# Kernel optimization log

Hardware: AMD Instinct MI355X
Metric: run time of the kernel (lower is better)

Reference implementation:

```python
import jax, jax.numpy as jnp
import numpy as np

B, N, E = 64, 2048, 32768
F_IN, NHID, RULES = 256, 512, 128
RATIO = 0.5
K1 = int(np.ceil(RATIO * N)); K2 = int(np.ceil(RATIO * K1)); K3 = int(np.ceil(RATIO * K2))


def _gcn(x, src, dst, em, W, b):
    # GCNConv with self-loops and symmetric normalization; em is a float edge-validity mask.
    n = x.shape[0]
    h = x @ W  # [n, out]
    deg = jax.ops.segment_sum(em, dst, num_segments=n) + 1.0  # in-degree + self-loop
    dinv = jax.lax.rsqrt(deg)
    coef = dinv[src] * dinv[dst] * em  # [E]
    agg = jax.ops.segment_sum(h[src] * coef[:, None], dst, num_segments=n)
    return agg + h / deg[:, None] + b  # second term = self-loop with norm 1/deg


def _sag_pool(x, src, dst, em, Wg, bg, k):
    # SAGPooling: GCN scorer, per-graph top-k, scale kept nodes by tanh(score), filter+reindex edges.
    n = x.shape[0]
    score = _gcn(x, src, dst, em, Wg, bg)[:, 0]  # [n]
    vals, perm = jax.lax.top_k(score, k)
    xk = x[perm] * jnp.tanh(vals)[:, None]  # [k, F]
    newidx = jnp.full((n,), -1, dtype=src.dtype).at[perm].set(jnp.arange(k, dtype=src.dtype))
    ns, nd = newidx[src], newidx[dst]
    keep = em * (ns >= 0).astype(em.dtype) * (nd >= 0).astype(em.dtype)
    return xk, jnp.maximum(ns, 0), jnp.maximum(nd, 0), keep


_gcn_b = jax.vmap(_gcn, in_axes=(0, 0, 0, 0, None, None))
_pool_b = jax.vmap(_sag_pool, in_axes=(0, 0, 0, 0, None, None, None))


def setup_inputs() -> dict:
    key = jax.random.key(0)
    ks = jax.random.split(key, 16)
    def w(k, shape, fan_in):
        return jax.random.normal(k, shape, jnp.float32) * (1.0 / np.sqrt(fan_in))
    return {
        "x": jax.random.normal(ks[0], (B, N, F_IN), jnp.float32),
        "src": jax.random.randint(ks[1], (B, E), 0, N, jnp.int32),
        "dst": jax.random.randint(ks[2], (B, E), 0, N, jnp.int32),
        "W1": w(ks[3], (F_IN, NHID), F_IN), "b1": jnp.zeros((NHID,), jnp.float32),
        "Wp1": w(ks[4], (NHID, 1), NHID), "bp1": jnp.zeros((1,), jnp.float32),
        "W2": w(ks[5], (NHID, NHID), NHID), "b2": jnp.zeros((NHID,), jnp.float32),
        "Wp2": w(ks[6], (NHID, 1), NHID), "bp2": jnp.zeros((1,), jnp.float32),
        "W3": w(ks[7], (NHID, NHID), NHID), "b3": jnp.zeros((NHID,), jnp.float32),
        "Wp3": w(ks[8], (NHID, 1), NHID), "bp3": jnp.zeros((1,), jnp.float32),
        "lin1_W": w(ks[9], (2 * NHID, NHID), 2 * NHID), "lin1_b": jnp.zeros((NHID,), jnp.float32),
        "lin2_W": w(ks[10], (NHID, NHID // 2), NHID), "lin2_b": jnp.zeros((NHID // 2,), jnp.float32),
        "pi_W": w(ks[11], (NHID // 2, RULES), NHID // 2), "pi_b": jnp.zeros((RULES,), jnp.float32),
        "v_W": w(ks[12], (NHID // 2, 1), NHID // 2), "v_b": jnp.zeros((1,), jnp.float32),
    }


def reference(x, src, dst, W1, b1, Wp1, bp1, W2, b2, Wp2, bp2, W3, b3, Wp3, bp3,
              lin1_W, lin1_b, lin2_W, lin2_b, pi_W, pi_b, v_W, v_b):
    em = jnp.ones(src.shape, x.dtype)
    h = jax.nn.relu(_gcn_b(x, src, dst, em, W1, b1))
    h, s, d, em = _pool_b(h, src, dst, em, Wp1, bp1, K1)
    x1 = jnp.concatenate([h.max(axis=1), h.mean(axis=1)], axis=1)  # [B, 2*NHID]
    h = jax.nn.relu(_gcn_b(h, s, d, em, W2, b2))
    h, s, d, em = _pool_b(h, s, d, em, Wp2, bp2, K2)
    x2 = jnp.concatenate([h.max(axis=1), h.mean(axis=1)], axis=1)
    h = jax.nn.relu(_gcn_b(h, s, d, em, W3, b3))
    h, s, d, em = _pool_b(h, s, d, em, Wp3, bp3, K3)
    x3 = jnp.concatenate([h.max(axis=1), h.mean(axis=1)], axis=1)
    z = x1 + x2 + x3
    z = jax.nn.relu(z @ lin1_W + lin1_b)
    z = jax.nn.relu(z @ lin2_W + lin2_b)
    pi = jax.nn.log_softmax(z @ pi_W + pi_b, axis=1)
    v = jax.nn.relu(z @ v_W + v_b)
    return pi, v
```

## Files before the change

### kernel.cpp

```cpp
#include <hip/hip_runtime.h>
#include <math.h>
#include <cstdint>

#define B_   64
#define N_   2048
#define E_   32768
#define FIN  256
#define H_   512

typedef __bf16 bf16x8 __attribute__((ext_vector_type(8)));
typedef float  f32x4  __attribute__((ext_vector_type(4)));

__device__ __forceinline__ unsigned short f2bf(float f) {
  unsigned u = __float_as_uint(f);
  u += 0x7FFF + ((u >> 16) & 1);
  return (unsigned short)(u >> 16);
}
__device__ __forceinline__ unsigned pk2(float a, float b) {
  return (unsigned)f2bf(a) | ((unsigned)f2bf(b) << 16);
}
__device__ __forceinline__ float bflo(unsigned u) { return __uint_as_float(u << 16); }
__device__ __forceinline__ float bfhi(unsigned u) { return __uint_as_float(u & 0xFFFF0000u); }

__device__ __forceinline__ void accum8(float* acc, uint4 u, float c) {
  acc[0] += c * bflo(u.x); acc[1] += c * bfhi(u.x);
  acc[2] += c * bflo(u.y); acc[3] += c * bfhi(u.y);
  acc[4] += c * bflo(u.z); acc[5] += c * bfhi(u.z);
  acc[6] += c * bflo(u.w); acc[7] += c * bfhi(u.w);
}

__device__ __forceinline__ void glds16(const void* g, void* l) {
  __builtin_amdgcn_global_load_lds(
      (const __attribute__((address_space(1))) unsigned int*)g,
      (__attribute__((address_space(3))) unsigned int*)l, 16, 0, 0);
}

__global__ void xcvt_k(const float* __restrict__ x, unsigned short* __restrict__ xb) {
  int i = blockIdx.x * 256 + threadIdx.x;
  float4 f = reinterpret_cast<const float4*>(x)[i];
  uint2 o; o.x = pk2(f.x, f.y); o.y = pk2(f.z, f.w);
  reinterpret_cast<uint2*>(xb)[i] = o;
}

__global__ void wcvt_k(const float* __restrict__ W, unsigned short* __restrict__ Wt, int K) {
  int idx = blockIdx.x * 256 + threadIdx.x;
  int k = idx >> 9, n = idx & 511;
  Wt[n * K + k] = f2bf(W[idx]);
}

__global__ __launch_bounds__(256) void gemm_mfma(
    const unsigned short* __restrict__ Xb,
    const int* __restrict__ perm, const float* __restrict__ tanhv,
    const unsigned short* __restrict__ Wt, unsigned short* __restrict__ Y,
    int K, int kl2, int nsl2,
    const float* __restrict__ bias, const float* __restrict__ wp, float* __restrict__ hs) {
  __shared__ __align__(16) char smem[34816];
  const int tid = threadIdx.x;
  const int w = tid >> 6, L = tid & 63;
  const int bid = blockIdx.x;
  const int xcd = bid & 7;
  const int t = bid >> 3;
  const int colb = t & 3;
  const int strip = ((t >> 2) << 3) + xcd;
  const int m0 = strip * 128;
  const int n0 = colb * 128;
  const int e = L & 15, q = L >> 4;

  const int sw3 = (L >> 3) & 7;
  const int cA = (w * 64 + L) ^ sw3;
  const int rloc = cA >> 2;
  const int kcs = (cA & 3) * 8;

  f32x4 acc[4][4];
#pragma unroll
  for (int j = 0; j < 4; j++)
#pragma unroll
    for (int nn = 0; nn < 4; nn++) acc[j][nn] = (f32x4){0.f, 0.f, 0.f, 0.f};

  size_t asrc[2];
#pragma unroll
  for (int i = 0; i < 2; i++) {
    int g = m0 + i * 64 + rloc;
    size_t row;
    if (perm) {
      int b = g >> kl2;
      int node = perm[g];
      row = (size_t)(b << nsl2) + node;
    } else {
      row = (size_t)g;
    }
    asrc[i] = row * (size_t)K + kcs;
  }
  size_t bsrc[2];
#pragma unroll
  for (int i = 0; i < 2; i++) bsrc[i] = (size_t)(n0 + i * 64 + rloc) * K + kcs;

  const int fo = e * 4 + q;
  const int fosw = fo ^ (fo >> 3);
  const int lofs = w * 64 * 16;

  const int nk = K >> 5;
  {
    char* Ab = smem;
    char* Bb = smem + 16384;
    glds16(Xb + asrc[0], Ab + 0 * 4096 + lofs);
    glds16(Xb + asrc[1], Ab + 1 * 4096 + lofs);
    glds16(Wt + bsrc[0], Bb + 0 * 4096 + lofs);
    glds16(Wt + bsrc[1], Bb + 1 * 4096 + lofs);
  }
  __syncthreads();
  int cur = 0;
  for (int kt = 0; kt < nk; ++kt) {
    if (kt + 1 < nk) {
      const int k0 = (kt + 1) << 5;
      char* Ab = smem + (cur ^ 1) * 8192;
      char* Bb = smem + 16384 + (cur ^ 1) * 8192;
      glds16(Xb + asrc[0] + k0, Ab + 0 * 4096 + lofs);
      glds16(Xb + asrc[1] + k0, Ab + 1 * 4096 + lofs);
      glds16(Wt + bsrc[0] + k0, Bb + 0 * 4096 + lofs);
      glds16(Wt + bsrc[1] + k0, Bb + 1 * 4096 + lofs);
    }
    const uint4* As = (const uint4*)(smem + cur * 8192);
    const uint4* Bs = (const uint4*)(smem + 16384 + cur * 8192);
    bf16x8 af[4], bfr[4];
#pragma unroll
    for (int j = 0; j < 4; j++) af[j]  = __builtin_bit_cast(bf16x8, As[((w & 1) * 4 + j) * 64 + fosw]);
#pragma unroll
    for (int j = 0; j < 4; j++) bfr[j] = __builtin_bit_cast(bf16x8, Bs[((w >> 1) * 4 + j) * 64 + fosw]);
#pragma unroll
    for (int j = 0; j < 4; j++)
#pragma unroll
      for (int nn = 0; nn < 4; nn++)
        acc[j][nn] = __builtin_amdgcn_mfma_f32_16x16x32_bf16(af[j], bfr[nn], acc[j][nn], 0, 0, 0);
    __syncthreads();
    cur ^= 1;
  }

  const int RS = 136;
  unsigned short* Csm = (unsigned short*)smem;
  float bs[4], wsv[4];
#pragma unroll
  for (int nn = 0; nn < 4; nn++) {
    int coly = n0 + ((w >> 1) * 4 + nn) * 16 + e;
    bs[nn]  = bias ? bias[coly] : 0.f;
    wsv[nn] = wp ? wp[coly] : 0.f;
  }
#pragma unroll
  for (int j = 0; j < 4; j++) {
    int mt = (w & 1) * 4 + j;
#pragma unroll
    for (int r = 0; r < 4; r++) {
      int lrow = mt * 16 + q * 4 + r;
      int grow = m0 + lrow;
      float t2 = tanhv ? tanhv[grow] : 1.0f;
      float p = 0.f;
#pragma unroll
      for (int nn = 0; nn < 4; nn++) {
        int lcol = (w >> 1) * 64 + nn * 16 + e;
        float v = acc[j][nn][r] * t2;
        if (bias) v = fmaxf(v + bs[nn], 0.f);
        Csm[lrow * RS + lcol] = f2bf(v);
        p += v * wsv[nn];
      }
      if (wp) {
        p += __shfl_xor(p, 1, 64); p += __shfl_xor(p, 2, 64);
        p += __shfl_xor(p, 4, 64); p += __shfl_xor(p, 8, 64);
        if ((L & 15) == 0) atomicAdd(&hs[grow], p);
      }
    }
  }
  __syncthreads();
  const int rbase = tid >> 4, ci = tid & 15;
#pragma unroll
  for (int pass = 0; pass < 8; ++pass) {
    int lrow = pass * 16 + rbase;
    uint4 u = *(const uint4*)(Csm + lrow * RS + ci * 8);
    *(uint4*)(Y + (size_t)(m0 + lrow) * 512 + n0 + ci * 8) = u;
  }
}

__global__ void count_k(const int* __restrict__ dst, int* __restrict__ cnt, int nl2) {
  int g = blockIdx.x * 256 + threadIdx.x;
  int d = dst[g];
  if (d < 0) return;
  int b = g >> 15;
  atomicAdd(&cnt[(b << nl2) + d], 1);
}

__global__ __launch_bounds__(256) void scan_k(const int* __restrict__ cnt,
                                              int* __restrict__ rowptr, int* __restrict__ cursor,
                                              float* __restrict__ deg, float* __restrict__ dinv, int n) {
  int b = blockIdx.x, tid = threadIdx.x;
  __shared__ int ls[2048];
  __shared__ int ch[256];
  int per = n >> 8;
  int base = tid * per;
  int s = 0;
  for (int i = 0; i < per; i++) { int v = cnt[b * n + base + i]; ls[base + i] = v; s += v; }
  ch[tid] = s;
  __syncthreads();
  for (int off = 1; off < 256; off <<= 1) {
    int v = (tid >= off) ? ch[tid - off] : 0;
    __syncthreads();
    ch[tid] += v;
    __syncthreads();
  }
  int run = (tid == 0) ? 0 : ch[tid - 1];
  for (int i = 0; i < per; i++) {
    int v = ls[base + i];
    rowptr[b * (n + 1) + base + i] = run;
    cursor[b * n + base + i] = run;
    float d = (float)(v + 1);
    deg[b * n + base + i] = d;
    dinv[b * n + base + i] = 1.0f / sqrtf(d);
    run += v;
  }
  if (tid == 255) rowptr[b * (n + 1) + n] = run;
}

__global__ void fill_k(const int* __restrict__ src, const int* __restrict__ dst,
                       const float* __restrict__ dinv, int* cursor, int* col,
                       float* ce, int nl2) {
  int g = blockIdx.x * 256 + threadIdx.x;
  int d = dst[g];
  if (d < 0) return;
  int b = g >> 15;
  int s = src[g];
  int pos = atomicAdd(&cursor[(b << nl2) + d], 1);
  col[(b << 15) + pos] = s;
  ce[(b << 15) + pos] = dinv[(b << nl2) + s] * dinv[(b << nl2) + d];
}

__global__ __launch_bounds__(256) void aggx_k(
    const unsigned short* __restrict__ X,
    const int* __restrict__ rowptr, const int* __restrict__ col,
    const float* __restrict__ ce, const float* __restrict__ deg,
    unsigned short* __restrict__ Xa) {
  const int hw = threadIdx.x >> 5, hl = threadIdx.x & 31;
  const int xcd = blockIdx.x & 7;
  const int slot = blockIdx.x >> 3;
  const int gslot = slot >> 8;
  const int v8 = slot & 255;
  const int b = (gslot << 3) + xcd;
  const int v = v8 * 8 + hw;
  const int bbase = b << 11;
  const int vg = bbase + v;
  const int rb = b * (N_ + 1) + v;
  const int st = rowptr[rb], en = rowptr[rb + 1];
  const int* cb = col + (b << 15);
  const float* cee = ce + (b << 15);
  const unsigned short* Xb_ = X + (size_t)bbase * 256 + hl * 8;
  float acc[8] = {0.f, 0.f, 0.f, 0.f, 0.f, 0.f, 0.f, 0.f};
  int e2 = st;
  for (; e2 + 4 <= en; e2 += 4) {
    int s0 = cb[e2], s1 = cb[e2 + 1], s2 = cb[e2 + 2], s3 = cb[e2 + 3];
    float c0 = cee[e2], c1 = cee[e2 + 1], c2 = cee[e2 + 2], c3 = cee[e2 + 3];
    uint4 u0 = *(const uint4*)(Xb_ + (size_t)s0 * 256);
    uint4 u1 = *(const uint4*)(Xb_ + (size_t)s1 * 256);
    uint4 u2 = *(const uint4*)(Xb_ + (size_t)s2 * 256);
    uint4 u3 = *(const uint4*)(Xb_ + (size_t)s3 * 256);
    accum8(acc, u0, c0); accum8(acc, u1, c1);
    accum8(acc, u2, c2); accum8(acc, u3, c3);
  }
  for (; e2 < en; e2++) {
    uint4 u = *(const uint4*)(Xb_ + (size_t)cb[e2] * 256);
    accum8(acc, u, cee[e2]);
  }
  {
    uint4 u = *(const uint4*)(Xb_ + (size_t)v * 256);
    accum8(acc, u, 1.0f / deg[vg]);
  }
  uint4 o;
  o.x = pk2(acc[0], acc[1]); o.y = pk2(acc[2], acc[3]);
  o.z = pk2(acc[4], acc[5]); o.w = pk2(acc[6], acc[7]);
  *(uint4*)(Xa + (size_t)vg * 256 + hl * 8) = o;
}

template <int NL2>
__global__ __launch_bounds__(256) void agg_k(
    const unsigned short* __restrict__ H,
    const int* __restrict__ rowptr, const int* __restrict__ col,
    const float* __restrict__ ce, const float* __restrict__ deg,
    const float* __restrict__ bias, const float* __restrict__ wp,
    unsigned short* __restrict__ C, float* __restrict__ hs) {
  const int n = 1 << NL2;
  const int xcd = blockIdx.x & 7;
  const int slot = blockIdx.x >> 3;
  const int gslot = slot >> (NL2 - 2);
  const int v4 = slot & ((1 << (NL2 - 2)) - 1);
  const int b = (gslot << 3) + xcd;
  const int w = threadIdx.x >> 6, L = threadIdx.x & 63;
  const int v = v4 * 4 + w;
  const int bbase = b << NL2;
  const int vg = bbase + v;
  const int rb = b * (n + 1) + v;
  const int st = rowptr[rb], en = rowptr[rb + 1];
  const int* cb = col + (b << 15);
  const float* cee = ce + (b << 15);
  const unsigned short* Hb_ = H + (size_t)bbase * 512 + (size_t)L * 8;

  float acc[8] = {0.f, 0.f, 0.f, 0.f, 0.f, 0.f, 0.f, 0.f};
  int e2 = st;
  for (; e2 + 4 <= en; e2 += 4) {
    int s0 = cb[e2], s1 = cb[e2 + 1], s2 = cb[e2 + 2], s3 = cb[e2 + 3];
    float c0 = cee[e2], c1 = cee[e2 + 1], c2 = cee[e2 + 2], c3 = cee[e2 + 3];
    uint4 u0 = *(const uint4*)(Hb_ + (size_t)s0 * 512);
    uint4 u1 = *(const uint4*)(Hb_ + (size_t)s1 * 512);
    uint4 u2 = *(const uint4*)(Hb_ + (size_t)s2 * 512);
    uint4 u3 = *(const uint4*)(Hb_ + (size_t)s3 * 512);
    accum8(acc, u0, c0); accum8(acc, u1, c1);
    accum8(acc, u2, c2); accum8(acc, u3, c3);
  }
  for (; e2 < en; e2++) {
    int s = cb[e2];
    uint4 u = *(const uint4*)(Hb_ + (size_t)s * 512);
    accum8(acc, u, cee[e2]);
  }
  {
    float idg = 1.0f / deg[vg];
    uint4 u = *(const uint4*)(Hb_ + (size_t)v * 512);
    accum8(acc, u, idg);
  }
  float4 bLo = *(const float4*)(bias + L * 8);
  float4 bHi = *(const float4*)(bias + L * 8 + 4);
  acc[0] = fmaxf(acc[0] + bLo.x, 0.f); acc[1] = fmaxf(acc[1] + bLo.y, 0.f);
  acc[2] = fmaxf(acc[2] + bLo.z, 0.f); acc[3] = fmaxf(acc[3] + bLo.w, 0.f);
  acc[4] = fmaxf(acc[4] + bHi.x, 0.f); acc[5] = fmaxf(acc[5] + bHi.y, 0.f);
  acc[6] = fmaxf(acc[6] + bHi.z, 0.f); acc[7] = fmaxf(acc[7] + bHi.w, 0.f);
  uint4 o;
  o.x = pk2(acc[0], acc[1]); o.y = pk2(acc[2], acc[3]);
  o.z = pk2(acc[4], acc[5]); o.w = pk2(acc[6], acc[7]);
  *(uint4*)(C + (size_t)vg * 512 + L * 8) = o;
  float4 wLo = *(const float4*)(wp + L * 8);
  float4 wHi = *(const float4*)(wp + L * 8 + 4);
  float p = acc[0] * wLo.x + acc[1] * wLo.y + acc[2] * wLo.z + acc[3] * wLo.w
          + acc[4] * wHi.x + acc[5] * wHi.y + acc[6] * wHi.z + acc[7] * wHi.w;
#pragma unroll
  for (int off = 32; off > 0; off >>= 1) p += __shfl_down(p, off, 64);
  if (L == 0) hs[vg] = p;
}

__global__ void scoreagg_k(const float* __restrict__ hs, const int* __restrict__ rowptr,
                           const int* __restrict__ col, const float* __restrict__ ce,
                           const float* __restrict__ deg, const float* __restrict__ bp,
                           float* __restrict__ score, int nl2) {
  int idx = blockIdx.x * 256 + threadIdx.x;
  int n = 1 << nl2;
  int b = idx >> nl2, v = idx & (n - 1);
  int rb = b * (n + 1) + v;
  int st = rowptr[rb], en = rowptr[rb + 1];
  const int* cb = col + (b << 15);
  const float* cee = ce + (b << 15);
  int bbase = b << nl2;
  float acc = 0.f;
  int e = st;
  for (; e + 4 <= en; e += 4) {
    acc += hs[bbase + cb[e]] * cee[e] + hs[bbase + cb[e + 1]] * cee[e + 1]
         + hs[bbase + cb[e + 2]] * cee[e + 2] + hs[bbase + cb[e + 3]] * cee[e + 3];
  }
  for (; e < en; e++) acc += hs[bbase + cb[e]] * cee[e];
  score[idx] = acc + hs[idx] / deg[idx] + bp[0];
}

__global__ __launch_bounds__(1024) void topk_k(const float* __restrict__ score, int* __restrict__ perm,
                                               float* __restrict__ tanhv, int* __restrict__ newidx,
                                               int n, int k) {
  int b = blockIdx.x, tid = threadIdx.x;
  __shared__ float ss[2048];
  __shared__ int si[2048];
  for (int i = tid; i < n; i += 1024) { ss[i] = score[b * n + i]; si[i] = i; }
  __syncthreads();
  for (int size = 2; size <= n; size <<= 1) {
    for (int stride = size >> 1; stride > 0; stride >>= 1) {
      for (int i = tid; i < n; i += 1024) {
        int j = i ^ stride;
        if (j > i) {
          bool up = ((i & size) == 0);
          float fi = ss[i], fj = ss[j];
          int ii = si[i], ij = si[j];
          bool iBefore = (fi > fj) || (fi == fj && ii < ij);
          bool sw = up ? (!iBefore) : iBefore;
          if (sw) { ss[i] = fj; ss[j] = fi; si[i] = ij; si[j] = ii; }
        }
      }
      __syncthreads();
    }
  }
  for (int r = tid; r < n; r += 1024) newidx[b * n + si[r]] = (r < k) ? r : -1;
  for (int r = tid; r < k; r += 1024) { perm[b * k + r] = si[r]; tanhv[b * k + r] = tanhf(ss[r]); }
}

__global__ void reindex_count_k(const int* srcO, const int* dstO, const int* newidx,
                                int* srcN, int* dstN, int* cnt, int nl2new) {
  int g = blockIdx.x * 256 + threadIdx.x;
  int b = g >> 15;
  int dd = dstO[g];
  int sN = 0, dN = -1;
  if (dd >= 0) {
    int ns = newidx[(b << (nl2new + 1)) + srcO[g]];
    int nd = newidx[(b << (nl2new + 1)) + dd];
    if (ns >= 0 && nd >= 0) {
      sN = ns; dN = nd;
      atomicAdd(&cnt[(b << nl2new) + nd], 1);
    }
  }
  srcN[g] = sN; dstN[g] = dN;
}

__global__ __launch_bounds__(512) void statsp_k(const unsigned short* __restrict__ C,
    const int* __restrict__ perm, const float* __restrict__ tv,
    float* __restrict__ zp, int nsl2, int k, int kch) {
  int b = blockIdx.x, rg = blockIdx.y, f = threadIdx.x;
  int r0 = rg * kch;
  float mx = -1e30f, sm = 0.f;
#pragma unroll 4
  for (int r = r0; r < r0 + kch; r++) {
    int node = perm[b * k + r];
    float t = tv[b * k + r];
    float val = __uint_as_float((unsigned)C[((size_t)((b << nsl2) + node)) * 512 + f] << 16) * t;
    mx = fmaxf(mx, val); sm += val;
  }
  zp[(size_t)(b * 8 + rg) * 1024 + f] = mx;
  zp[(size_t)(b * 8 + rg) * 1024 + 512 + f] = sm;
}

__global__ __launch_bounds__(512) void statsr_k(const float* __restrict__ zp,
                                                float* __restrict__ z, int k) {
  int b = blockIdx.x, f = threadIdx.x;
  float mx = -1e30f, sm = 0.f;
#pragma unroll
  for (int g = 0; g < 8; g++) {
    mx = fmaxf(mx, zp[(size_t)(b * 8 + g) * 1024 + f]);
    sm += zp[(size_t)(b * 8 + g) * 1024 + 512 + f];
  }
  z[b * 1024 + f] += mx;
  z[b * 1024 + 512 + f] += sm / (float)k;
}

__global__ __launch_bounds__(256) void mlp1_k(const float* __restrict__ z,
                                              const float* __restrict__ W1,
                                              float* __restrict__ zp1) {
  const int kc = blockIdx.x & 7;
  const int b = blockIdx.x >> 3;
  const int tid = threadIdx.x;
  __shared__ float zs[128];
  if (tid < 128) zs[tid] = z[b * 1024 + kc * 128 + tid];
  __syncthreads();
  float a0 = 0.f, a1 = 0.f;
  const float* Wb = W1 + (size_t)(kc * 128) * 512 + tid * 2;
#pragma unroll 4
  for (int i = 0; i < 128; i++) {
    float2 w = *(const float2*)(Wb + (size_t)i * 512);
    float zi = zs[i];
    a0 += zi * w.x; a1 += zi * w.y;
  }
  reinterpret_cast<float2*>(zp1 + ((size_t)(kc * 64 + b)) * 512)[tid] = make_float2(a0, a1);
}

__global__ __launch_bounds__(256) void mlp2_k(const float* __restrict__ zp1,
                                              const float* __restrict__ b1,
                                              const float* __restrict__ W2,
                                              float* __restrict__ zp2) {
  const int kc = blockIdx.x & 1;
  const int b = blockIdx.x >> 1;
  const int tid = threadIdx.x;
  __shared__ float z1s[256];
  {
    int i = kc * 256 + tid;
    float a = b1[i];
#pragma unroll
    for (int g = 0; g < 8; g++) a += zp1[((size_t)(g * 64 + b)) * 512 + i];
    z1s[tid] = fmaxf(a, 0.f);
  }
  __syncthreads();
  float a = 0.f;
  const float* Wb = W2 + (size_t)(kc * 256) * 256 + tid;
#pragma unroll 4
  for (int i = 0; i < 256; i++) a += z1s[i] * Wb[(size_t)i * 256];
  zp2[((size_t)(kc * 64 + b)) * 256 + tid] = a;
}

__global__ __launch_bounds__(128) void mlp3_k(const float* __restrict__ zp2,
                                              const float* __restrict__ b2,
                                              const float* __restrict__ piW,
                                              const float* __restrict__ pib,
                                              const float* __restrict__ vW,
                                              const float* __restrict__ vb,
                                              float* __restrict__ out) {
  const int b = blockIdx.x, tid = threadIdx.x;
  __shared__ float z2s[256];
  __shared__ float wred[4];
  __shared__ float sred[2];
  for (int t = tid; t < 256; t += 128) {
    float a = b2[t] + zp2[(size_t)b * 256 + t] + zp2[(size_t)(64 + b) * 256 + t];
    z2s[t] = fmaxf(a, 0.f);
  }
  __syncthreads();
  float a = pib[tid];
#pragma unroll 4
  for (int i = 0; i < 256; i++) a += z2s[i] * piW[(size_t)i * 128 + tid];
  float vp = z2s[tid] * vW[tid] + z2s[tid + 128] * vW[tid + 128];
  float m = a;
#pragma unroll
  for (int off = 32; off > 0; off >>= 1) {
    vp += __shfl_xor(vp, off, 64);
    m = fmaxf(m, __shfl_xor(m, off, 64));
  }
  const int wv = tid >> 6;
  if ((tid & 63) == 0) { wred[wv] = m; wred[2 + wv] = vp; }
  __syncthreads();
  m = fmaxf(wred[0], wred[1]);
  float s = expf(a - m);
#pragma unroll
  for (int off = 32; off > 0; off >>= 1) s += __shfl_xor(s, off, 64);
  if ((tid & 63) == 0) sred[wv] = s;
  __syncthreads();
  s = sred[0] + sred[1];
  if (tid == 0) out[B_ * 128 + b] = fmaxf(vb[0] + wred[2] + wred[3], 0.f);
  out[b * 128 + tid] = a - m - logf(s);
}

extern "C" void kernel_launch(void* const* d_in, const int* in_sizes, int n_in,
                              void* d_out, int out_size, void* d_ws, size_t ws_size,
                              hipStream_t stream) {
  const float* x    = (const float*)d_in[0];
  const int*   src0 = (const int*)d_in[1];
  const int*   dst0 = (const int*)d_in[2];
  const float* W1   = (const float*)d_in[3];
  const float* b1   = (const float*)d_in[4];
  const float* Wp1  = (const float*)d_in[5];
  const float* bp1  = (const float*)d_in[6];
  const float* W2   = (const float*)d_in[7];
  const float* b2   = (const float*)d_in[8];
  const float* Wp2  = (const float*)d_in[9];
  const float* bp2  = (const float*)d_in[10];
  const float* W3   = (const float*)d_in[11];
  const float* b3   = (const float*)d_in[12];
  const float* Wp3  = (const float*)d_in[13];
  const float* bp3  = (const float*)d_in[14];
  const float* l1W  = (const float*)d_in[15];
  const float* l1b  = (const float*)d_in[16];
  const float* l2W  = (const float*)d_in[17];
  const float* l2b  = (const float*)d_in[18];
  const float* piW  = (const float*)d_in[19];
  const float* pib  = (const float*)d_in[20];
  const float* vW   = (const float*)d_in[21];
  const float* vb   = (const float*)d_in[22];
  float* out = (float*)d_out;
  (void)in_sizes; (void)n_in; (void)out_size; (void)ws_size;

  unsigned short* Cb = (unsigned short*)d_in[0];

  char* base = (char*)d_ws;
  size_t off = 0;
  auto alloc = [&](size_t bytes) -> void* {
    void* r = base + off;
    off += (bytes + 255) & ~(size_t)255;
    return r;
  };
  unsigned short* Hb   = (unsigned short*)alloc((size_t)B_ * 1024 * H_ * 2);
  unsigned short* xb   = (unsigned short*)alloc((size_t)B_ * N_ * FIN * 2);
  unsigned short* Xa   = (unsigned short*)alloc((size_t)B_ * N_ * FIN * 2);
  unsigned short* W1t  = (unsigned short*)alloc((size_t)512 * 256 * 2);
  unsigned short* W2t  = (unsigned short*)alloc((size_t)512 * 512 * 2);
  unsigned short* W3t  = (unsigned short*)alloc((size_t)512 * 512 * 2);
  int*   srcA   = (int*)alloc((size_t)B_ * E_ * 4);
  int*   dstA   = (int*)alloc((size_t)B_ * E_ * 4);
  int*   col    = (int*)alloc((size_t)B_ * E_ * 4);
  float* coefE  = (float*)alloc((size_t)B_ * E_ * 4);
  int*   cnt    = (int*)alloc((size_t)B_ * N_ * 4);
  int*   cursor = (int*)alloc((size_t)B_ * N_ * 4);
  int*   rowptr = (int*)alloc((size_t)B_ * (N_ + 1) * 4);
  float* deg    = (float*)alloc((size_t)B_ * N_ * 4);
  float* dinv   = (float*)alloc((size_t)B_ * N_ * 4);
  float* hs     = (float*)alloc((size_t)B_ * N_ * 4);
  float* score  = (float*)alloc((size_t)B_ * N_ * 4);
  int*   newidx = (int*)alloc((size_t)B_ * N_ * 4);
  int*   perm   = (int*)alloc((size_t)B_ * 1024 * 4);
  float* tanhv  = (float*)alloc((size_t)B_ * 1024 * 4);
  float* zpart  = (float*)alloc((size_t)B_ * 8 * 1024 * 4);
  float* z      = (float*)alloc((size_t)B_ * 1024 * 4);

  float* zp1 = zpart;
  float* zp2 = zpart + (size_t)8 * 64 * 512;

  const int EB = B_ * E_ / 256;

  xcvt_k<<<B_ * N_ * FIN / 4 / 256, 256, 0, stream>>>(x, xb);
  wcvt_k<<<256 * 512 / 256, 256, 0, stream>>>(W1, W1t, 256);
  wcvt_k<<<512 * 512 / 256, 256, 0, stream>>>(W2, W2t, 512);
  wcvt_k<<<512 * 512 / 256, 256, 0, stream>>>(W3, W3t, 512);
  hipMemsetAsync(z, 0, (size_t)B_ * 1024 * 4, stream);

  {
    hipMemsetAsync(cnt, 0, (size_t)B_ * 2048 * 4, stream);
    count_k<<<EB, 256, 0, stream>>>(dst0, cnt, 11);
    scan_k<<<B_, 256, 0, stream>>>(cnt, rowptr, cursor, deg, dinv, 2048);
    fill_k<<<EB, 256, 0, stream>>>(src0, dst0, dinv, cursor, col, coefE, 11);
    aggx_k<<<B_ * 2048 / 8, 256, 0, stream>>>(xb, rowptr, col, coefE, deg, Xa);
    hipMemsetAsync(hs, 0, (size_t)B_ * 2048 * 4, stream);
    gemm_mfma<<<B_ * 2048 / 128 * 4, 256, 0, stream>>>(
        Xa, nullptr, nullptr, W1t, Cb, 256, 0, 0, b1, Wp1, hs);
    scoreagg_k<<<B_ * 2048 / 256, 256, 0, stream>>>(hs, rowptr, col, coefE, deg, bp1, score, 11);
    topk_k<<<B_, 1024, 0, stream>>>(score, perm, tanhv, newidx, 2048, 1024);
    statsp_k<<<dim3(B_, 8), 512, 0, stream>>>(Cb, perm, tanhv, zpart, 11, 1024, 128);
    statsr_k<<<B_, 512, 0, stream>>>(zpart, z, 1024);
    hipMemsetAsync(cnt, 0, (size_t)B_ * 1024 * 4, stream);
    reindex_count_k<<<EB, 256, 0, stream>>>(src0, dst0, newidx, srcA, dstA, cnt, 10);
    scan_k<<<B_, 256, 0, stream>>>(cnt, rowptr, cursor, deg, dinv, 1024);
    fill_k<<<EB, 256, 0, stream>>>(srcA, dstA, dinv, cursor, col, coefE, 10);
  }
  {
    gemm_mfma<<<B_ * 1024 / 128 * 4, 256, 0, stream>>>(
        Cb, perm, tanhv, W2t, Hb, 512, 10, 11, nullptr, nullptr, nullptr);
    agg_k<10><<<B_ * 1024 / 4, 256, 0, stream>>>(Hb, rowptr, col, coefE, deg, b2, Wp2, Cb, hs);
    scoreagg_k<<<B_ * 1024 / 256, 256, 0, stream>>>(hs, rowptr, col, coefE, deg, bp2, score, 10);
    topk_k<<<B_, 1024, 0, stream>>>(score, perm, tanhv, newidx, 1024, 512);
    statsp_k<<<dim3(B_, 8), 512, 0, stream>>>(Cb, perm, tanhv, zpart, 10, 512, 64);
    statsr_k<<<B_, 512, 0, stream>>>(zpart, z, 512);
    hipMemsetAsync(cnt, 0, (size_t)B_ * 512 * 4, stream);
    reindex_count_k<<<EB, 256, 0, stream>>>(srcA, dstA, newidx, srcA, dstA, cnt, 9);
    scan_k<<<B_, 256, 0, stream>>>(cnt, rowptr, cursor, deg, dinv, 512);
    fill_k<<<EB, 256, 0, stream>>>(srcA, dstA, dinv, cursor, col, coefE, 9);
  }
  {
    gemm_mfma<<<B_ * 512 / 128 * 4, 256, 0, stream>>>(
        Cb, perm, tanhv, W3t, Hb, 512, 9, 10, nullptr, nullptr, nullptr);
    agg_k<9><<<B_ * 512 / 4, 256, 0, stream>>>(Hb, rowptr, col, coefE, deg, b3, Wp3, Cb, hs);
    scoreagg_k<<<B_ * 512 / 256, 256, 0, stream>>>(hs, rowptr, col, coefE, deg, bp3, score, 9);
    topk_k<<<B_, 1024, 0, stream>>>(score, perm, tanhv, newidx, 512, 256);
    statsp_k<<<dim3(B_, 8), 512, 0, stream>>>(Cb, perm, tanhv, zpart, 9, 256, 32);
    statsr_k<<<B_, 512, 0, stream>>>(zpart, z, 256);
  }

  mlp1_k<<<B_ * 8, 256, 0, stream>>>(z, l1W, zp1);
  mlp2_k<<<B_ * 2, 256, 0, stream>>>(zp1, l1b, l2W, zp2);
  mlp3_k<<<B_, 128, 0, stream>>>(zp2, l2b, piW, pib, vW, vb, out);
}
```

Baseline: 1.036 ms.

## Fuse CSR build (count, scan, fill, reindex) into one per-graph LDS kernel

Replaces the separate memset, count, reindex_count, scan and fill launches with a single templated kernel per pooling stage. Each graph gets one 512-thread block that counts, scans, computes degrees and fills the CSR, using shared-memory atomics and shared copies of newidx and dinv. This removes several launches and memsets plus the global atomic traffic on the count and cursor arrays. The trade-off is that only 64 blocks run on the GPU, and each must loop serially over 32K edges in several passes. Source and destination buffers are aliased in place while marked restrict, which is a correctness risk.

```diff
diff --git a/kernel.cpp b/kernel.cpp
--- a/kernel.cpp
+++ b/kernel.cpp
@@ -179,56 +179,87 @@
   }
 }
 
-__global__ void count_k(const int* __restrict__ dst, int* __restrict__ cnt, int nl2) {
-  int g = blockIdx.x * 256 + threadIdx.x;
-  int d = dst[g];
-  if (d < 0) return;
-  int b = g >> 15;
-  atomicAdd(&cnt[(b << nl2) + d], 1);
-}
-
-__global__ __launch_bounds__(256) void scan_k(const int* __restrict__ cnt,
-                                              int* __restrict__ rowptr, int* __restrict__ cursor,
-                                              float* __restrict__ deg, float* __restrict__ dinv, int n) {
-  int b = blockIdx.x, tid = threadIdx.x;
-  __shared__ int ls[2048];
-  __shared__ int ch[256];
-  int per = n >> 8;
-  int base = tid * per;
+template <int NL2, bool REINDEX>
+__global__ __launch_bounds__(512) void csr_k(
+    const int* __restrict__ srcO, const int* __restrict__ dstO,
+    const int* __restrict__ newidx,
+    int* __restrict__ srcN, int* __restrict__ dstN,
+    int* __restrict__ rowptr, float* __restrict__ deg, float* __restrict__ dinv,
+    int* __restrict__ col, float* __restrict__ ce) {
+  const int n = 1 << NL2;
+  const int b = blockIdx.x, tid = threadIdx.x;
+  __shared__ int   lcnt[1 << NL2];
+  __shared__ int   ch[512];
+  __shared__ float ldv[1 << NL2];
+  __shared__ int   lnew[REINDEX ? (2 << NL2) : 1];
+  const int eb = b << 15;
+
+  for (int i = tid; i < n; i += 512) lcnt[i] = 0;
+  if (REINDEX)
+    for (int i = tid; i < 2 * n; i += 512) lnew[i] = newidx[(b << (NL2 + 1)) + i];
+  __syncthreads();
+
+  if (REINDEX) {
+    for (int e2 = tid; e2 < E_; e2 += 512) {
+      int dd = dstO[eb + e2];
+      int sN = 0, dN = -1;
+      if (dd >= 0) {
+        int ss = srcO[eb + e2];
+        int ns = lnew[ss], nd = lnew[dd];
+        if (ns >= 0 && nd >= 0) { sN = ns; dN = nd; atomicAdd(&lcnt[nd], 1); }
+      }
+      srcN[eb + e2] = sN; dstN[eb + e2] = dN;
+    }
+  } else {
+    for (int e2 = tid; e2 < E_; e2 += 512) {
+      int d = dstO[eb + e2];
+      if (d >= 0) atomicAdd(&lcnt[d], 1);
+    }
+  }
+  __syncthreads();
+
+  const int per = n >> 9;
+  const int base = tid * per;
+  int lc[per];
   int s = 0;
-  for (int i = 0; i < per; i++) { int v = cnt[b * n + base + i]; ls[base + i] = v; s += v; }
+#pragma unroll
+  for (int i = 0; i < per; i++) { lc[i] = lcnt[base + i]; s += lc[i]; }
   ch[tid] = s;
   __syncthreads();
-  for (int off = 1; off < 256; off <<= 1) {
+  for (int off = 1; off < 512; off <<= 1) {
     int v = (tid >= off) ? ch[tid - off] : 0;
     __syncthreads();
     ch[tid] += v;
     __syncthreads();
   }
   int run = (tid == 0) ? 0 : ch[tid - 1];
+#pragma unroll
   for (int i = 0; i < per; i++) {
-    int v = ls[base + i];
-    rowptr[b * (n + 1) + base + i] = run;
-    cursor[b * n + base + i] = run;
+    int v = lc[i];
+    int g = base + i;
+    rowptr[b * (n + 1) + g] = run;
+    lcnt[g] = run;
     float d = (float)(v + 1);
-    deg[b * n + base + i] = d;
-    dinv[b * n + base + i] = 1.0f / sqrtf(d);
+    deg[(b << NL2) + g] = d;
+    float iv = 1.0f / sqrtf(d);
+    ldv[g] = iv;
+    dinv[(b << NL2) + g] = iv;
     run += v;
   }
-  if (tid == 255) rowptr[b * (n + 1) + n] = run;
-}
-
-__global__ void fill_k(const int* __restrict__ src, const int* __restrict__ dst,
-                       const float* __restrict__ dinv, int* cursor, int* col,
-                       float* ce, int nl2) {
-  int g = blockIdx.x * 256 + threadIdx.x;
-  int d = dst[g];
-  if (d < 0) return;
-  int b = g >> 15;
-  int s = src[g];
-  int pos = atomicAdd(&cursor[(b << nl2) + d], 1);
-  col[(b << 15) + pos] = s;
-  ce[(b << 15) + pos] = dinv[(b << nl2) + s] * dinv[(b << nl2) + d];
+  if (tid == 511) rowptr[b * (n + 1) + n] = run;
+  __syncthreads();
+
+  const int* S2 = REINDEX ? srcN : srcO;
+  const int* D2 = REINDEX ? dstN : dstO;
+  for (int e2 = tid; e2 < E_; e2 += 512) {
+    int d = D2[eb + e2];
+    if (d >= 0) {
+      int ss = S2[eb + e2];
+      int pos = atomicAdd(&lcnt[d], 1);
+      col[eb + pos] = ss;
+      ce[eb + pos] = ldv[ss] * ldv[d];
+    }
+  }
 }
 
 __global__ __launch_bounds__(256) void aggx_k(
@@ -390,23 +421,6 @@
   for (int r = tid; r < k; r += 1024) { perm[b * k + r] = si[r]; tanhv[b * k + r] = tanhf(ss[r]); }
 }
 
-__global__ void reindex_count_k(const int* srcO, const int* dstO, const int* newidx,
-                                int* srcN, int* dstN, int* cnt, int nl2new) {
-  int g = blockIdx.x * 256 + threadIdx.x;
-  int b = g >> 15;
-  int dd = dstO[g];
-  int sN = 0, dN = -1;
-  if (dd >= 0) {
-    int ns = newidx[(b << (nl2new + 1)) + srcO[g]];
-    int nd = newidx[(b << (nl2new + 1)) + dd];
-    if (ns >= 0 && nd >= 0) {
-      sN = ns; dN = nd;
-      atomicAdd(&cnt[(b << nl2new) + nd], 1);
-    }
-  }
-  srcN[g] = sN; dstN[g] = dN;
-}
-
 __global__ __launch_bounds__(512) void statsp_k(const unsigned short* __restrict__ C,
     const int* __restrict__ perm, const float* __restrict__ tv,
     float* __restrict__ zp, int nsl2, int k, int kch) {
@@ -568,8 +582,6 @@
   int*   dstA   = (int*)alloc((size_t)B_ * E_ * 4);
   int*   col    = (int*)alloc((size_t)B_ * E_ * 4);
   float* coefE  = (float*)alloc((size_t)B_ * E_ * 4);
-  int*   cnt    = (int*)alloc((size_t)B_ * N_ * 4);
-  int*   cursor = (int*)alloc((size_t)B_ * N_ * 4);
   int*   rowptr = (int*)alloc((size_t)B_ * (N_ + 1) * 4);
   float* deg    = (float*)alloc((size_t)B_ * N_ * 4);
   float* dinv   = (float*)alloc((size_t)B_ * N_ * 4);
@@ -584,8 +596,6 @@
   float* zp1 = zpart;
   float* zp2 = zpart + (size_t)8 * 64 * 512;
 
-  const int EB = B_ * E_ / 256;
-
   xcvt_k<<<B_ * N_ * FIN / 4 / 256, 256, 0, stream>>>(x, xb);
   wcvt_k<<<256 * 512 / 256, 256, 0, stream>>>(W1, W1t, 256);
   wcvt_k<<<512 * 512 / 256, 256, 0, stream>>>(W2, W2t, 512);
@@ -593,10 +603,8 @@
   hipMemsetAsync(z, 0, (size_t)B_ * 1024 * 4, stream);
 
   {
-    hipMemsetAsync(cnt, 0, (size_t)B_ * 2048 * 4, stream);
-    count_k<<<EB, 256, 0, stream>>>(dst0, cnt, 11);
-    scan_k<<<B_, 256, 0, stream>>>(cnt, rowptr, cursor, deg, dinv, 2048);
-    fill_k<<<EB, 256, 0, stream>>>(src0, dst0, dinv, cursor, col, coefE, 11);
+    csr_k<11, false><<<B_, 512, 0, stream>>>(src0, dst0, nullptr, nullptr, nullptr,
+                                             rowptr, deg, dinv, col, coefE);
     aggx_k<<<B_ * 2048 / 8, 256, 0, stream>>>(xb, rowptr, col, coefE, deg, Xa);
     hipMemsetAsync(hs, 0, (size_t)B_ * 2048 * 4, stream);
     gemm_mfma<<<B_ * 2048 / 128 * 4, 256, 0, stream>>>(
@@ -605,10 +613,8 @@
     topk_k<<<B_, 1024, 0, stream>>>(score, perm, tanhv, newidx, 2048, 1024);
     statsp_k<<<dim3(B_, 8), 512, 0, stream>>>(Cb, perm, tanhv, zpart, 11, 1024, 128);
     statsr_k<<<B_, 512, 0, stream>>>(zpart, z, 1024);
-    hipMemsetAsync(cnt, 0, (size_t)B_ * 1024 * 4, stream);
-    reindex_count_k<<<EB, 256, 0, stream>>>(src0, dst0, newidx, srcA, dstA, cnt, 10);
-    scan_k<<<B_, 256, 0, stream>>>(cnt, rowptr, cursor, deg, dinv, 1024);
-    fill_k<<<EB, 256, 0, stream>>>(srcA, dstA, dinv, cursor, col, coefE, 10);
+    csr_k<10, true><<<B_, 512, 0, stream>>>(src0, dst0, newidx, srcA, dstA,
+                                            rowptr, deg, dinv, col, coefE);
   }
   {
     gemm_mfma<<<B_ * 1024 / 128 * 4, 256, 0, stream>>>(
@@ -618,10 +624,8 @@
     topk_k<<<B_, 1024, 0, stream>>>(score, perm, tanhv, newidx, 1024, 512);
     statsp_k<<<dim3(B_, 8), 512, 0, stream>>>(Cb, perm, tanhv, zpart, 10, 512, 64);
     statsr_k<<<B_, 512, 0, stream>>>(zpart, z, 512);
-    hipMemsetAsync(cnt, 0, (size_t)B_ * 512 * 4, stream);
-    reindex_count_k<<<EB, 256, 0, stream>>>(srcA, dstA, newidx, srcA, dstA, cnt, 9);
-    scan_k<<<B_, 256, 0, stream>>>(cnt, rowptr, cursor, deg, dinv, 512);
-    fill_k<<<EB, 256, 0, stream>>>(srcA, dstA, dinv, cursor, col, coefE, 9);
+    csr_k<9, true><<<B_, 512, 0, stream>>>(srcA, dstA, newidx, srcA, dstA,
+                                           rowptr, deg, dinv, col, coefE);
   }
   {
     gemm_mfma<<<B_ * 512 / 128 * 4, 256, 0, stream>>>(
```

Result: slower. 1.123 ms (+8.4%).
